# Kernel tuning notes

Measured on AMD Instinct MI355X. Metric: run time of the kernel, lower is better.

The kernel has to match this reference:

```python
import jax, jax.numpy as jnp
import numpy as np

N = 100000  # nodes per type (user, tweet)
E = 500000  # edges per relation
D = 128     # input feature dim
H = 128     # hidden dim


def _seg_mean(h_src, src, dst, n_dst):
    # DGL copy_u + mean: mean of source features over incoming edges; zero for in-degree 0.
    msg = h_src[src]                                                    # [E, F] gather
    s = jax.ops.segment_sum(msg, dst, num_segments=n_dst)               # [n_dst, F] scatter-add
    cnt = jax.ops.segment_sum(jnp.ones((src.shape[0], 1), h_src.dtype), dst, num_segments=n_dst)
    return s / jnp.maximum(cnt, 1.0)


def setup_inputs() -> dict:
    key = jax.random.key(0)
    ks = jax.random.split(key, 24)
    f = lambda i, shp, s=1.0: jax.random.normal(ks[i], shp, dtype=jnp.float32) * s
    return {
        'x_user': f(0, (N, D)), 'x_tweet': f(1, (N, D)),
        # layer 1, relation 'posts' (user -> tweet) and 'posted_by' (tweet -> user)
        'w1ps': f(2, (H, D), 0.05), 'b1ps': f(3, (H,), 0.05),
        'w1pn': f(4, (H, D), 0.05), 'b1pn': f(5, (H,), 0.05),
        'w1bs': f(6, (H, D), 0.05), 'b1bs': f(7, (H,), 0.05),
        'w1bn': f(8, (H, D), 0.05), 'b1bn': f(9, (H,), 0.05),
        # layer 2 (out_feats = 1, no activation)
        'w2ps': f(10, (1, H), 0.05), 'b2ps': f(11, (1,), 0.05),
        'w2pn': f(12, (1, H), 0.05), 'b2pn': f(13, (1,), 0.05),
        'w2bs': f(14, (1, H), 0.05), 'b2bs': f(15, (1,), 0.05),
        'w2bn': f(16, (1, H), 0.05), 'b2bn': f(17, (1,), 0.05),
        'src_posts': jax.random.randint(ks[18], (E,), 0, N),
        'dst_posts': jax.random.randint(ks[19], (E,), 0, N),
        'src_pb': jax.random.randint(ks[20], (E,), 0, N),
        'dst_pb': jax.random.randint(ks[21], (E,), 0, N),
    }


def reference(x_user, x_tweet,
              w1ps, b1ps, w1pn, b1pn, w1bs, b1bs, w1bn, b1bn,
              w2ps, b2ps, w2pn, b2pn, w2bs, b2bs, w2bn, b2bn,
              src_posts, dst_posts, src_pb, dst_pb):
    # ---- conv1: DivFeatConv per relation, relu, cross-relation sum (one rel per dst type) ----
    neigh_t = _seg_mean(x_user, src_posts, dst_posts, N)               # user -posts-> tweet
    h_tweet = jax.nn.relu(x_tweet @ w1ps.T + b1ps + neigh_t @ w1pn.T + b1pn)
    neigh_u = _seg_mean(x_tweet, src_pb, dst_pb, N)                    # tweet -posted_by-> user
    h_user = jax.nn.relu(x_user @ w1bs.T + b1bs + neigh_u @ w1bn.T + b1bn)
    # ---- conv2: out_feats=1, identity activation ----
    neigh_t2 = _seg_mean(h_user, src_posts, dst_posts, N)
    out_tweet = h_tweet @ w2ps.T + b2ps + neigh_t2 @ w2pn.T + b2pn     # [N, 1]
    neigh_u2 = _seg_mean(h_tweet, src_pb, dst_pb, N)
    out_user = h_user @ w2bs.T + b2bs + neigh_u2 @ w2bn.T + b2bn       # [N, 1]
    return (out_user, out_tweet)
```

## Files before the change

### kernel.cpp

```cpp
#include <hip/hip_runtime.h>

#define N_NODES 100000
#define N_EDGES 500000
#define DIM 128
#define GB_E 1954
#define GB_N 391
#define GB_CVT 12500
#define GB_G 782
#define GB_SEG 6250

typedef __attribute__((ext_vector_type(8))) short short8;
typedef __attribute__((ext_vector_type(4))) float f32x4;

__device__ __forceinline__ ushort f2bf(float f) {
    unsigned u = __float_as_uint(f);
    u += 0x7FFF + ((u >> 16) & 1);
    return (ushort)(u >> 16);
}
__device__ __forceinline__ float bf2f(ushort s) {
    return __uint_as_float(((unsigned)s) << 16);
}


__device__ __forceinline__ void build_body(const int* __restrict__ src,
                                           const int* __restrict__ dst,
                                           int* __restrict__ head,
                                           int2* __restrict__ entry, int bid) {
    int e = bid * 256 + threadIdx.x;
    if (e < N_EDGES) {
        int d = dst[e];
        int old = atomicExch(&head[d], e);
        entry[e] = make_int2(src[e], old);
    }
}

__device__ __forceinline__ void cvt_body(const float* __restrict__ in,
                                         ushort* __restrict__ out, int bid) {
    int i = (bid * 256 + threadIdx.x) * 4;
    float4 v = *reinterpret_cast<const float4*>(&in[i]);
    ushort4 u = make_ushort4(f2bf(v.x), f2bf(v.y), f2bf(v.z), f2bf(v.w));
    *reinterpret_cast<ushort4*>(&out[i]) = u;
}

__device__ __forceinline__ void seg_body(const ushort* __restrict__ x,
                                         const int* __restrict__ head,
                                         const int2* __restrict__ entry,
                                         ushort* __restrict__ outbf, int bid) {
    int idx = bid * 256 + threadIdx.x;
    int node = idx >> 4;
    if (node >= N_NODES) return;
    int f = (idx & 15) << 3;
    float acc[8];
#pragma unroll
    for (int j = 0; j < 8; ++j) acc[j] = 0.f;
    int cnt = 0;
    int e = head[node];
    while (e >= 0) {
        int2 nd = entry[e];
        ++cnt;
        short8 v = *reinterpret_cast<const short8*>(&x[(size_t)nd.x * DIM + f]);
#pragma unroll
        for (int j = 0; j < 8; ++j) acc[j] += bf2f((ushort)v[j]);
        e = nd.y;
    }
    float r = 1.0f / fmaxf((float)cnt, 1.0f);
    union { ushort s[8]; uint4 v; } u;
#pragma unroll
    for (int j = 0; j < 8; ++j) u.s[j] = f2bf(acc[j] * r);
    *reinterpret_cast<uint4*>(&outbf[(size_t)node * DIM + f]) = u.v;
}

__device__ __forceinline__ float smean_body(const float* __restrict__ sval,
                                            const int* __restrict__ head,
                                            const int2* __restrict__ entry, int node) {
    float a = 0.f;
    int cnt = 0;
    int e = head[node];
    while (e >= 0) {
        int2 nd = entry[e];
        ++cnt;
        a += sval[nd.x];
        e = nd.y;
    }
    return a / fmaxf((float)cnt, 1.0f);
}

__device__ __forceinline__ void gemm_body(
    const ushort* __restrict__ Xsbf, const ushort* __restrict__ Nm,
    const ushort* __restrict__ Wsbf, const ushort* __restrict__ Wnbf,
    const float* __restrict__ bs, const float* __restrict__ bn,
    const float* __restrict__ w2a, const float* __restrict__ w2b,
    float* __restrict__ dself, float* __restrict__ dcross, int blk) {
    __shared__ ushort sA[128 * 64];
    __shared__ ushort sB[128 * 64];
    __shared__ float pS[2][2][128];

    const int tid = threadIdx.x;
    const int lane = tid & 63;
    const int wid = tid >> 6;
    const int wr = wid >> 1, wc = wid & 1;
    const int lr = lane & 15, lg = lane >> 4;
    const int row0 = blk * 128;

    f32x4 acc[4][4];
#pragma unroll
    for (int i = 0; i < 4; ++i)
#pragma unroll
        for (int j = 0; j < 4; ++j) acc[i][j] = (f32x4){0.f, 0.f, 0.f, 0.f};

    const int r = tid >> 1;
    const int hh = tid & 1;
    const int grow = row0 + r;
    const int swzr = (r & 7) << 4;

    for (int kb = 0; kb < 256; kb += 64) {
        const int kg = kb & 127;
        const bool self = (kb < 128);
        __syncthreads();
        {
            const uint4* g = reinterpret_cast<const uint4*>(self ? Xsbf : Nm);
#pragma unroll
            for (int q = 0; q < 4; ++q) {
                uint4 v = make_uint4(0, 0, 0, 0);
                if (grow < N_NODES)
                    v = g[((size_t)grow * DIM + kg + hh * 32 + q * 8) >> 3];
                int byte = (hh * 64 + q * 16) ^ swzr;
                *reinterpret_cast<uint4*>(&sA[r * 64 + (byte >> 1)]) = v;
            }
        }
        {
            const uint4* g = reinterpret_cast<const uint4*>(self ? Wsbf : Wnbf);
#pragma unroll
            for (int q = 0; q < 4; ++q) {
                uint4 v = g[(r * DIM + kg + hh * 32 + q * 8) >> 3];
                int byte = (hh * 64 + q * 16) ^ swzr;
                *reinterpret_cast<uint4*>(&sB[r * 64 + (byte >> 1)]) = v;
            }
        }
        __syncthreads();
#pragma unroll
        for (int ks = 0; ks < 2; ++ks) {
            short8 a[4], b[4];
#pragma unroll
            for (int fm = 0; fm < 4; ++fm) {
                int rr = wr * 64 + fm * 16 + lr;
                int byte = (ks * 64 + lg * 16) ^ ((rr & 7) << 4);
                a[fm] = *reinterpret_cast<const short8*>(&sA[rr * 64 + (byte >> 1)]);
            }
#pragma unroll
            for (int fn = 0; fn < 4; ++fn) {
                int cc = wc * 64 + fn * 16 + lr;
                int byte = (ks * 64 + lg * 16) ^ ((cc & 7) << 4);
                b[fn] = *reinterpret_cast<const short8*>(&sB[cc * 64 + (byte >> 1)]);
            }
#pragma unroll
            for (int fm = 0; fm < 4; ++fm)
#pragma unroll
                for (int fn = 0; fn < 4; ++fn)
                    acc[fm][fn] = __builtin_amdgcn_mfma_f32_16x16x32_bf16(
                        a[fm], b[fn], acc[fm][fn], 0, 0, 0);
        }
    }

    float bias[4], wa[4], wb[4];
#pragma unroll
    for (int fn = 0; fn < 4; ++fn) {
        int c = wc * 64 + fn * 16 + lr;
        bias[fn] = bs[c] + bn[c];
        wa[fn] = w2a[c];
        wb[fn] = w2b[c];
    }
#pragma unroll
    for (int fm = 0; fm < 4; ++fm) {
#pragma unroll
        for (int reg = 0; reg < 4; ++reg) {
            float pa = 0.f, pb = 0.f;
#pragma unroll
            for (int fn = 0; fn < 4; ++fn) {
                float h = fmaxf(acc[fm][fn][reg] + bias[fn], 0.f);
                pa = fmaf(h, wa[fn], pa);
                pb = fmaf(h, wb[fn], pb);
            }
#pragma unroll
            for (int m = 1; m < 16; m <<= 1) {
                pa += __shfl_xor(pa, m);
                pb += __shfl_xor(pb, m);
            }
            if (lr == 0) {
                int rloc = wr * 64 + fm * 16 + lg * 4 + reg;
                pS[wc][0][rloc] = pa;
                pS[wc][1][rloc] = pb;
            }
        }
    }
    __syncthreads();
    if (tid < 128) {
        int go = row0 + tid;
        if (go < N_NODES) {
            dself[go] = pS[0][0][tid] + pS[1][0][tid];
            dcross[go] = pS[0][1][tid] + pS[1][1][tid];
        }
    }
}


__global__ __launch_bounds__(256) void fatA_kernel(
    const int* __restrict__ sp, const int* __restrict__ dp,
    const int* __restrict__ sb, const int* __restrict__ db,
    int* __restrict__ head2, int2* __restrict__ entry2,
    const float* __restrict__ w0, const float* __restrict__ w1,
    const float* __restrict__ w2, const float* __restrict__ w3,
    ushort* __restrict__ o0, ushort* __restrict__ o1,
    ushort* __restrict__ o2, ushort* __restrict__ o3,
    const float* __restrict__ xu, const float* __restrict__ xt,
    ushort* __restrict__ xbf_u, ushort* __restrict__ xbf_t) {
    int bid = blockIdx.x;
    if (bid < 2 * GB_E) {
        int rel = (bid >= GB_E);
        build_body(rel ? sb : sp, rel ? db : dp, head2 + (size_t)rel * N_NODES,
                   entry2 + (size_t)rel * N_EDGES, bid - rel * GB_E);
    } else if (bid < 2 * GB_E + 64) {
        int b = bid - 2 * GB_E;
        int a = b >> 4;
        const float* in = (a == 0) ? w0 : (a == 1) ? w1 : (a == 2) ? w2 : w3;
        ushort* out = (a == 0) ? o0 : (a == 1) ? o1 : (a == 2) ? o2 : o3;
        cvt_body(in, out, b & 15);
    } else {
        int b = bid - 2 * GB_E - 64;
        int which = (b >= GB_CVT);
        cvt_body(which ? xt : xu, which ? xbf_t : xbf_u, b - which * GB_CVT);
    }
}

__global__ __launch_bounds__(256) void seg_only_kernel(
    const ushort* __restrict__ x, const int* __restrict__ head,
    const int2* __restrict__ entry, ushort* __restrict__ outbf) {
    seg_body(x, head, entry, outbf, blockIdx.x);
}

__global__ __launch_bounds__(256) void fatB_kernel(
    const ushort* __restrict__ xbf_t, const ushort* __restrict__ nbf0,
    const ushort* __restrict__ wbf_ps, const ushort* __restrict__ wbf_pn,
    const float* __restrict__ b1ps, const float* __restrict__ b1pn,
    const float* __restrict__ w2ps, const float* __restrict__ w2bn,
    float* __restrict__ dself_t, float* __restrict__ scross_t,
    const int* __restrict__ head_pb, const int2* __restrict__ ent_pb,
    ushort* __restrict__ nbf1) {
    int bid = blockIdx.x;
    if (bid < GB_G)
        gemm_body(xbf_t, nbf0, wbf_ps, wbf_pn, b1ps, b1pn, w2ps, w2bn,
                  dself_t, scross_t, bid);
    else
        seg_body(xbf_t, head_pb, ent_pb, nbf1, bid - GB_G);
}

__global__ __launch_bounds__(256) void fatC_kernel(
    const ushort* __restrict__ xbf_u, const ushort* __restrict__ nbf1,
    const ushort* __restrict__ wbf_bs, const ushort* __restrict__ wbf_bn,
    const float* __restrict__ b1bs, const float* __restrict__ b1bn,
    const float* __restrict__ w2bs, const float* __restrict__ w2pn,
    float* __restrict__ dself_u, float* __restrict__ scross_u,
    const float* __restrict__ scross_t,
    const int* __restrict__ head_pb, const int2* __restrict__ ent_pb,
    float* __restrict__ smean_u) {
    int bid = blockIdx.x;
    if (bid < GB_G) {
        gemm_body(xbf_u, nbf1, wbf_bs, wbf_bn, b1bs, b1bn, w2bs, w2pn,
                  dself_u, scross_u, bid);
    } else {
        int i = (bid - GB_G) * 256 + threadIdx.x;
        if (i < N_NODES) smean_u[i] = smean_body(scross_t, head_pb, ent_pb, i);
    }
}

__global__ __launch_bounds__(256) void tail_kernel(
    const float* __restrict__ dself_u, const float* __restrict__ smean_u,
    const float* __restrict__ dself_t, const float* __restrict__ scross_u,
    const int* __restrict__ head_posts, const int2* __restrict__ ent_posts,
    const float* __restrict__ b2bs, const float* __restrict__ b2bn,
    const float* __restrict__ b2ps, const float* __restrict__ b2pn,
    float* __restrict__ out) {
    int i = blockIdx.x * 256 + threadIdx.x;
    if (i >= N_NODES) return;
    out[N_NODES + i] = dself_t[i] + smean_body(scross_u, head_posts, ent_posts, i)
                       + b2ps[0] + b2pn[0];
    out[i] = dself_u[i] + smean_u[i] + b2bs[0] + b2bn[0];
}


__global__ __launch_bounds__(256) void cvtw_kernel(
    const float* __restrict__ w0, const float* __restrict__ w1,
    const float* __restrict__ w2, const float* __restrict__ w3,
    ushort* __restrict__ o0, ushort* __restrict__ o1,
    ushort* __restrict__ o2, ushort* __restrict__ o3) {
    int a = blockIdx.y;
    const float* in = (a == 0) ? w0 : (a == 1) ? w1 : (a == 2) ? w2 : w3;
    ushort* out = (a == 0) ? o0 : (a == 1) ? o1 : (a == 2) ? o2 : o3;
    cvt_body(in, out, blockIdx.x);
}

__global__ __launch_bounds__(256) void build_lists2_kernel(
    const int* __restrict__ s0, const int* __restrict__ d0,
    const int* __restrict__ s1, const int* __restrict__ d1,
    int* __restrict__ head2, int2* __restrict__ entry2) {
    const int rel = blockIdx.y;
    build_body(rel ? s1 : s0, rel ? d1 : d0, head2 + (size_t)rel * N_NODES,
               entry2 + (size_t)rel * N_EDGES, blockIdx.x);
}

__global__ __launch_bounds__(256) void seg_mean_f32_list_kernel(
    const float* __restrict__ x, const int* __restrict__ head,
    const int2* __restrict__ entry, ushort* __restrict__ outbf) {
    int idx = blockIdx.x * 256 + threadIdx.x;
    int node = idx >> 5;
    if (node >= N_NODES) return;
    int f = (idx & 31) << 2;
    float4 acc = make_float4(0.f, 0.f, 0.f, 0.f);
    int cnt = 0;
    int e = head[node];
    while (e >= 0) {
        int2 nd = entry[e];
        ++cnt;
        float4 v = *reinterpret_cast<const float4*>(&x[(size_t)nd.x * DIM + f]);
        acc.x += v.x; acc.y += v.y; acc.z += v.z; acc.w += v.w;
        e = nd.y;
    }
    float r = 1.0f / fmaxf((float)cnt, 1.0f);
    ushort4 u = make_ushort4(f2bf(acc.x * r), f2bf(acc.y * r),
                             f2bf(acc.z * r), f2bf(acc.w * r));
    *reinterpret_cast<ushort4*>(&outbf[node * DIM + f]) = u;
}

__global__ __launch_bounds__(256) void gemm_mfma_f32_kernel(
    const float* __restrict__ Xs, const ushort* __restrict__ Nm,
    const ushort* __restrict__ Wsbf, const ushort* __restrict__ Wnbf,
    const float* __restrict__ bs, const float* __restrict__ bn,
    const float* __restrict__ w2a, const float* __restrict__ w2b,
    float* __restrict__ dself, float* __restrict__ dcross) {
    __shared__ ushort sA[128 * 64];
    __shared__ ushort sB[128 * 64];
    __shared__ float pS[2][2][128];

    const int tid = threadIdx.x;
    const int lane = tid & 63;
    const int wid = tid >> 6;
    const int wr = wid >> 1, wc = wid & 1;
    const int lr = lane & 15, lg = lane >> 4;
    const int row0 = blockIdx.x * 128;

    f32x4 acc[4][4];
#pragma unroll
    for (int i = 0; i < 4; ++i)
#pragma unroll
        for (int j = 0; j < 4; ++j) acc[i][j] = (f32x4){0.f, 0.f, 0.f, 0.f};

    const int r = tid >> 1;
    const int hh = tid & 1;
    const int grow = row0 + r;
    const int swzr = (r & 7) << 4;

    for (int kb = 0; kb < 256; kb += 64) {
        const int kg = kb & 127;
        const bool self = (kb < 128);
        __syncthreads();
        if (self) {
            const float4* g = reinterpret_cast<const float4*>(Xs);
#pragma unroll
            for (int q = 0; q < 4; ++q) {
                float4 v0 = make_float4(0.f, 0.f, 0.f, 0.f), v1 = v0;
                if (grow < N_NODES) {
                    size_t bi = ((size_t)grow * DIM + kg + hh * 32 + q * 8) >> 2;
                    v0 = g[bi];
                    v1 = g[bi + 1];
                }
                union { ushort s[8]; uint4 v; } u;
                u.s[0] = f2bf(v0.x); u.s[1] = f2bf(v0.y);
                u.s[2] = f2bf(v0.z); u.s[3] = f2bf(v0.w);
                u.s[4] = f2bf(v1.x); u.s[5] = f2bf(v1.y);
                u.s[6] = f2bf(v1.z); u.s[7] = f2bf(v1.w);
                int byte = (hh * 64 + q * 16) ^ swzr;
                *reinterpret_cast<uint4*>(&sA[r * 64 + (byte >> 1)]) = u.v;
            }
        } else {
            const uint4* g = reinterpret_cast<const uint4*>(Nm);
#pragma unroll
            for (int q = 0; q < 4; ++q) {
                uint4 v = make_uint4(0, 0, 0, 0);
                if (grow < N_NODES)
                    v = g[((size_t)grow * DIM + kg + hh * 32 + q * 8) >> 3];
                int byte = (hh * 64 + q * 16) ^ swzr;
                *reinterpret_cast<uint4*>(&sA[r * 64 + (byte >> 1)]) = v;
            }
        }
        {
            const uint4* g = reinterpret_cast<const uint4*>(self ? Wsbf : Wnbf);
#pragma unroll
            for (int q = 0; q < 4; ++q) {
                uint4 v = g[(r * DIM + kg + hh * 32 + q * 8) >> 3];
                int byte = (hh * 64 + q * 16) ^ swzr;
                *reinterpret_cast<uint4*>(&sB[r * 64 + (byte >> 1)]) = v;
            }
        }
        __syncthreads();
#pragma unroll
        for (int ks = 0; ks < 2; ++ks) {
            short8 a[4], b[4];
#pragma unroll
            for (int fm = 0; fm < 4; ++fm) {
                int rr = wr * 64 + fm * 16 + lr;
                int byte = (ks * 64 + lg * 16) ^ ((rr & 7) << 4);
                a[fm] = *reinterpret_cast<const short8*>(&sA[rr * 64 + (byte >> 1)]);
            }
#pragma unroll
            for (int fn = 0; fn < 4; ++fn) {
                int cc = wc * 64 + fn * 16 + lr;
                int byte = (ks * 64 + lg * 16) ^ ((cc & 7) << 4);
                b[fn] = *reinterpret_cast<const short8*>(&sB[cc * 64 + (byte >> 1)]);
            }
#pragma unroll
            for (int fm = 0; fm < 4; ++fm)
#pragma unroll
                for (int fn = 0; fn < 4; ++fn)
                    acc[fm][fn] = __builtin_amdgcn_mfma_f32_16x16x32_bf16(
                        a[fm], b[fn], acc[fm][fn], 0, 0, 0);
        }
    }

    float bias[4], wa[4], wb[4];
#pragma unroll
    for (int fn = 0; fn < 4; ++fn) {
        int c = wc * 64 + fn * 16 + lr;
        bias[fn] = bs[c] + bn[c];
        wa[fn] = w2a[c];
        wb[fn] = w2b[c];
    }
#pragma unroll
    for (int fm = 0; fm < 4; ++fm) {
#pragma unroll
        for (int reg = 0; reg < 4; ++reg) {
            float pa = 0.f, pb = 0.f;
#pragma unroll
            for (int fn = 0; fn < 4; ++fn) {
                float h = fmaxf(acc[fm][fn][reg] + bias[fn], 0.f);
                pa = fmaf(h, wa[fn], pa);
                pb = fmaf(h, wb[fn], pb);
            }
#pragma unroll
            for (int m = 1; m < 16; m <<= 1) {
                pa += __shfl_xor(pa, m);
                pb += __shfl_xor(pb, m);
            }
            if (lr == 0) {
                int rloc = wr * 64 + fm * 16 + lg * 4 + reg;
                pS[wc][0][rloc] = pa;
                pS[wc][1][rloc] = pb;
            }
        }
    }
    __syncthreads();
    if (tid < 128) {
        int go = row0 + tid;
        if (go < N_NODES) {
            dself[go] = pS[0][0][tid] + pS[1][0][tid];
            dcross[go] = pS[0][1][tid] + pS[1][1][tid];
        }
    }
}

__global__ __launch_bounds__(256) void scalar_finalize_kernel(
    const float* __restrict__ dself_u, const float* __restrict__ dself_t,
    const float* __restrict__ scross_u, const float* __restrict__ scross_t,
    const int* __restrict__ head2, const int2* __restrict__ entry2,
    const float* __restrict__ b2bs, const float* __restrict__ b2bn,
    const float* __restrict__ b2ps, const float* __restrict__ b2pn,
    float* __restrict__ out) {
    int i = blockIdx.x * 256 + threadIdx.x;
    if (i >= N_NODES) return;
    out[N_NODES + i] = dself_t[i] + smean_body(scross_u, head2, entry2, i)
                       + b2ps[0] + b2pn[0];
    out[i] = dself_u[i] + smean_body(scross_t, head2 + N_NODES, entry2 + N_EDGES, i)
             + b2bs[0] + b2bn[0];
}


extern "C" void kernel_launch(void* const* d_in, const int* in_sizes, int n_in,
                              void* d_out, int out_size, void* d_ws, size_t ws_size,
                              hipStream_t stream) {
    const float* x_user  = (const float*)d_in[0];
    const float* x_tweet = (const float*)d_in[1];
    const float* w1ps = (const float*)d_in[2];  const float* b1ps = (const float*)d_in[3];
    const float* w1pn = (const float*)d_in[4];  const float* b1pn = (const float*)d_in[5];
    const float* w1bs = (const float*)d_in[6];  const float* b1bs = (const float*)d_in[7];
    const float* w1bn = (const float*)d_in[8];  const float* b1bn = (const float*)d_in[9];
    const float* w2ps = (const float*)d_in[10]; const float* b2ps = (const float*)d_in[11];
    const float* w2pn = (const float*)d_in[12]; const float* b2pn = (const float*)d_in[13];
    const float* w2bs = (const float*)d_in[14]; const float* b2bs = (const float*)d_in[15];
    const float* w2bn = (const float*)d_in[16]; const float* b2bn = (const float*)d_in[17];
    const int* src_posts = (const int*)d_in[18];
    const int* dst_posts = (const int*)d_in[19];
    const int* src_pb    = (const int*)d_in[20];
    const int* dst_pb    = (const int*)d_in[21];
    float* out = (float*)d_out;

    char* wsb = (char*)d_ws;
    ushort* nbf0    = (ushort*)wsb;   wsb += (size_t)N_NODES * DIM * 2;
    int* head2      = (int*)wsb;      wsb += (size_t)2 * N_NODES * 4;
    int2* entry2    = (int2*)wsb;     wsb += (size_t)2 * N_EDGES * 8;
    ushort* wbf_ps  = (ushort*)wsb;   wsb += (size_t)DIM * DIM * 2;
    ushort* wbf_pn  = (ushort*)wsb;   wsb += (size_t)DIM * DIM * 2;
    ushort* wbf_bs  = (ushort*)wsb;   wsb += (size_t)DIM * DIM * 2;
    ushort* wbf_bn  = (ushort*)wsb;   wsb += (size_t)DIM * DIM * 2;
    float* dself_t  = (float*)wsb;    wsb += (size_t)N_NODES * 4;
    float* scross_t = (float*)wsb;    wsb += (size_t)N_NODES * 4;
    float* dself_u  = (float*)wsb;    wsb += (size_t)N_NODES * 4;
    float* scross_u = (float*)wsb;    wsb += (size_t)N_NODES * 4;
    float* smean_u  = (float*)wsb;    wsb += (size_t)N_NODES * 4;
    ushort* nbf1    = (ushort*)wsb;   wsb += (size_t)N_NODES * DIM * 2;
    ushort* xbf_u   = (ushort*)wsb;   wsb += (size_t)N_NODES * DIM * 2;
    ushort* xbf_t   = (ushort*)wsb;   wsb += (size_t)N_NODES * DIM * 2;
    const bool use_bf = ((size_t)(wsb - (char*)d_ws) <= ws_size);

    const int* head_posts = head2;
    const int* head_pb    = head2 + N_NODES;
    const int2* ent_posts = entry2;
    const int2* ent_pb    = entry2 + N_EDGES;

    hipMemsetAsync(head2, 0xFF, (size_t)2 * N_NODES * sizeof(int), stream);

    if (!use_bf) {
        cvtw_kernel<<<dim3(16, 4), 256, 0, stream>>>(w1ps, w1pn, w1bs, w1bn,
                                                     wbf_ps, wbf_pn, wbf_bs, wbf_bn);
        build_lists2_kernel<<<dim3(GB_E, 2), 256, 0, stream>>>(
            src_posts, dst_posts, src_pb, dst_pb, head2, entry2);
        seg_mean_f32_list_kernel<<<(N_NODES * 32 + 255) / 256, 256, 0, stream>>>(
            x_user, head_posts, ent_posts, nbf0);
        gemm_mfma_f32_kernel<<<GB_G, 256, 0, stream>>>(x_tweet, nbf0, wbf_ps, wbf_pn,
                                                       b1ps, b1pn, w2ps, w2bn,
                                                       dself_t, scross_t);
        seg_mean_f32_list_kernel<<<(N_NODES * 32 + 255) / 256, 256, 0, stream>>>(
            x_tweet, head_pb, ent_pb, nbf0);
        gemm_mfma_f32_kernel<<<GB_G, 256, 0, stream>>>(x_user, nbf0, wbf_bs, wbf_bn,
                                                       b1bs, b1bn, w2bs, w2pn,
                                                       dself_u, scross_u);
        scalar_finalize_kernel<<<GB_N, 256, 0, stream>>>(dself_u, dself_t,
                                                         scross_u, scross_t,
                                                         head2, entry2,
                                                         b2bs, b2bn, b2ps, b2pn, out);
        return;
    }

    fatA_kernel<<<2 * GB_E + 64 + 2 * GB_CVT, 256, 0, stream>>>(
        src_posts, dst_posts, src_pb, dst_pb, head2, entry2,
        w1ps, w1pn, w1bs, w1bn, wbf_ps, wbf_pn, wbf_bs, wbf_bn,
        x_user, x_tweet, xbf_u, xbf_t);

    seg_only_kernel<<<GB_SEG, 256, 0, stream>>>(xbf_u, head_posts, ent_posts, nbf0);

    fatB_kernel<<<GB_G + GB_SEG, 256, 0, stream>>>(
        xbf_t, nbf0, wbf_ps, wbf_pn, b1ps, b1pn, w2ps, w2bn,
        dself_t, scross_t, head_pb, ent_pb, nbf1);

    fatC_kernel<<<GB_G + GB_N, 256, 0, stream>>>(
        xbf_u, nbf1, wbf_bs, wbf_bn, b1bs, b1bn, w2bs, w2pn,
        dself_u, scross_u, scross_t, head_pb, ent_pb, smean_u);

    tail_kernel<<<GB_N, 256, 0, stream>>>(dself_u, smean_u, dself_t, scross_u,
                                          head_posts, ent_posts,
                                          b2bs, b2bn, b2ps, b2pn, out);
}
```

Baseline: 221.4 us.

## Overlap posted_by list build with posts segment-mean in a fused launch

The fused kernel that built both edge lists and converted inputs is split up. Conversion runs first, then the posts list is built alone, and the posted_by list build runs in the same launch as the posts segment-mean gather. This moves half of the atomic list-building work off the critical path by overlapping it with the memory-bound gather. The cost is one extra kernel launch and a different block mix that may contend for bandwidth.

```diff
diff --git a/kernel.cpp b/kernel.cpp
--- a/kernel.cpp
+++ b/kernel.cpp
@@ -204,10 +204,7 @@
 }
 
 
-__global__ __launch_bounds__(256) void fatA_kernel(
-    const int* __restrict__ sp, const int* __restrict__ dp,
-    const int* __restrict__ sb, const int* __restrict__ db,
-    int* __restrict__ head2, int2* __restrict__ entry2,
+__global__ __launch_bounds__(256) void cvt_fat_kernel(
     const float* __restrict__ w0, const float* __restrict__ w1,
     const float* __restrict__ w2, const float* __restrict__ w3,
     ushort* __restrict__ o0, ushort* __restrict__ o1,
@@ -215,27 +212,34 @@
     const float* __restrict__ xu, const float* __restrict__ xt,
     ushort* __restrict__ xbf_u, ushort* __restrict__ xbf_t) {
     int bid = blockIdx.x;
-    if (bid < 2 * GB_E) {
-        int rel = (bid >= GB_E);
-        build_body(rel ? sb : sp, rel ? db : dp, head2 + (size_t)rel * N_NODES,
-                   entry2 + (size_t)rel * N_EDGES, bid - rel * GB_E);
-    } else if (bid < 2 * GB_E + 64) {
-        int b = bid - 2 * GB_E;
-        int a = b >> 4;
+    if (bid < 64) {
+        int a = bid >> 4;
         const float* in = (a == 0) ? w0 : (a == 1) ? w1 : (a == 2) ? w2 : w3;
         ushort* out = (a == 0) ? o0 : (a == 1) ? o1 : (a == 2) ? o2 : o3;
-        cvt_body(in, out, b & 15);
+        cvt_body(in, out, bid & 15);
     } else {
-        int b = bid - 2 * GB_E - 64;
+        int b = bid - 64;
         int which = (b >= GB_CVT);
         cvt_body(which ? xt : xu, which ? xbf_t : xbf_u, b - which * GB_CVT);
     }
 }
 
-__global__ __launch_bounds__(256) void seg_only_kernel(
-    const ushort* __restrict__ x, const int* __restrict__ head,
-    const int2* __restrict__ entry, ushort* __restrict__ outbf) {
-    seg_body(x, head, entry, outbf, blockIdx.x);
+__global__ __launch_bounds__(256) void build1_kernel(
+    const int* __restrict__ src, const int* __restrict__ dst,
+    int* __restrict__ head, int2* __restrict__ entry) {
+    build_body(src, dst, head, entry, blockIdx.x);
+}
+
+__global__ __launch_bounds__(256) void fatS_kernel(
+    const int* __restrict__ s1, const int* __restrict__ d1,
+    int* __restrict__ head_pb, int2* __restrict__ ent_pb,
+    const ushort* __restrict__ xbf_u, const int* __restrict__ head_posts,
+    const int2* __restrict__ ent_posts, ushort* __restrict__ nbf0) {
+    int bid = blockIdx.x;
+    if (bid < GB_E)
+        build_body(s1, d1, head_pb, ent_pb, bid);
+    else
+        seg_body(xbf_u, head_posts, ent_posts, nbf0, bid - GB_E);
 }
 
 __global__ __launch_bounds__(256) void fatB_kernel(
@@ -520,10 +524,10 @@
     ushort* xbf_t   = (ushort*)wsb;   wsb += (size_t)N_NODES * DIM * 2;
     const bool use_bf = ((size_t)(wsb - (char*)d_ws) <= ws_size);
 
-    const int* head_posts = head2;
-    const int* head_pb    = head2 + N_NODES;
-    const int2* ent_posts = entry2;
-    const int2* ent_pb    = entry2 + N_EDGES;
+    int* head_posts = head2;
+    int* head_pb    = head2 + N_NODES;
+    int2* ent_posts = entry2;
+    int2* ent_pb    = entry2 + N_EDGES;
 
     hipMemsetAsync(head2, 0xFF, (size_t)2 * N_NODES * sizeof(int), stream);
 
@@ -549,12 +553,14 @@
         return;
     }
 
-    fatA_kernel<<<2 * GB_E + 64 + 2 * GB_CVT, 256, 0, stream>>>(
-        src_posts, dst_posts, src_pb, dst_pb, head2, entry2,
+    cvt_fat_kernel<<<64 + 2 * GB_CVT, 256, 0, stream>>>(
         w1ps, w1pn, w1bs, w1bn, wbf_ps, wbf_pn, wbf_bs, wbf_bn,
         x_user, x_tweet, xbf_u, xbf_t);
 
-    seg_only_kernel<<<GB_SEG, 256, 0, stream>>>(xbf_u, head_posts, ent_posts, nbf0);
+    build1_kernel<<<GB_E, 256, 0, stream>>>(src_posts, dst_posts, head_posts, ent_posts);
+
+    fatS_kernel<<<GB_E + GB_SEG, 256, 0, stream>>>(
+        src_pb, dst_pb, head_pb, ent_pb, xbf_u, head_posts, ent_posts, nbf0);
 
     fatB_kernel<<<GB_G + GB_SEG, 256, 0, stream>>>(
         xbf_t, nbf0, wbf_ps, wbf_pn, b1ps, b1pn, w2ps, w2bn,
```

New measurement: 218.5 us. No clear change (-1.3%).
